# Kernel tuning notes

Hardware: AMD Instinct MI355X
Metric: run time of the kernel (lower is better)

The kernel has to match this reference:

```python
import jax, jax.numpy as jnp
from jax import lax
import numpy as np

VOCAB = 50000
EMB = 256
HID = 512
NFEAT = 2048
B, T = 128, 64


def setup_inputs() -> dict:
    key = jax.random.key(0)
    ks = jax.random.split(key, 9)
    s_e = 1.0 / np.sqrt(HID)
    return {
        "m": jax.random.randint(ks[0], (B, T), 0, VOCAB, dtype=jnp.int64) if jax.config.jax_enable_x64 else jax.random.randint(ks[0], (B, T), 0, VOCAB, dtype=jnp.int32),
        "images": jax.random.normal(ks[1], (B, NFEAT), dtype=jnp.float32),
        "emb_table": jax.random.normal(ks[2], (VOCAB, EMB), dtype=jnp.float32),
        "W_ih": jax.random.uniform(ks[3], (4 * HID, EMB), jnp.float32, -s_e, s_e),
        "W_hh": jax.random.uniform(ks[4], (4 * HID, HID), jnp.float32, -s_e, s_e),
        "b_ih": jax.random.uniform(ks[5], (4 * HID,), jnp.float32, -s_e, s_e),
        "b_hh": jax.random.uniform(ks[6], (4 * HID,), jnp.float32, -s_e, s_e),
        "W_out": jax.random.uniform(ks[7], (NFEAT, HID), jnp.float32, -s_e, s_e),
        "b_out": jax.random.uniform(ks[8], (NFEAT,), jnp.float32, -s_e, s_e),
    }


def reference(m, images, emb_table, W_ih, W_hh, b_ih, b_hh, W_out, b_out):
    # m: [B, T] int token ids. images is unused by the original forward.
    Bsz = m.shape[0]
    emb = emb_table[m]                                  # [B, T, E]
    # Precompute input projections for all steps (one big GEMM)
    x_proj = jnp.einsum("bte,ge->btg", emb, W_ih) + b_ih  # [B, T, 4H]
    x_proj = jnp.swapaxes(x_proj, 0, 1)                   # [T, B, 4H]

    h0 = jnp.zeros((Bsz, HID), dtype=emb.dtype)
    c0 = jnp.zeros((Bsz, HID), dtype=emb.dtype)

    def step(carry, xg):
        h, c = carry
        gates = xg + h @ W_hh.T + b_hh                  # [B, 4H]
        i, f, g, o = jnp.split(gates, 4, axis=-1)       # PyTorch LSTMCell gate order
        c_new = jax.nn.sigmoid(f) * c + jax.nn.sigmoid(i) * jnp.tanh(g)
        h_new = jax.nn.sigmoid(o) * jnp.tanh(c_new)
        return (h_new, c_new), None

    (h, _), _ = lax.scan(step, (h0, c0), x_proj)
    return h @ W_out.T + b_out                           # [B, NFEAT]
```

## Files before the change

kernel.cpp:

```cpp
#include <hip/hip_runtime.h>
#include <hip/hip_bf16.h>

#define BATCH 128
#define TSTEPS 64
#define EMB 256
#define HID 512
#define GATES 2048
#define NFEAT 2048

typedef __bf16 bf16_t;
typedef __attribute__((ext_vector_type(8))) __bf16 bf16x8;
typedef __attribute__((ext_vector_type(4))) float f32x4;

#define MFMA16 __builtin_amdgcn_mfma_f32_16x16x32_bf16

__device__ __forceinline__ bf16x8 frag16(const bf16_t* __restrict__ base, int row0, int stride,
                                         int k0, int lane) {
    return *(const bf16x8*)(base + (size_t)(row0 + (lane & 15)) * stride + k0 + ((lane >> 4) << 3));
}

__device__ __forceinline__ float sigm(float x) { return 1.f / (1.f + __expf(-x)); }
__device__ __forceinline__ float tanh_f(float x) { return 1.f - 2.f / (__expf(2.f * x) + 1.f); }

__device__ __forceinline__ unsigned ld_sys(const unsigned* p) {
    return __hip_atomic_load(p, __ATOMIC_RELAXED, __HIP_MEMORY_SCOPE_SYSTEM);
}
__device__ __forceinline__ void st_sys(unsigned* p, unsigned v) {
    __hip_atomic_store(p, v, __ATOMIC_RELAXED, __HIP_MEMORY_SCOPE_SYSTEM);
}
__device__ __forceinline__ void ld2_sys_v4(const void* p0, const void* p1, uint4& a, uint4& b) {
    asm volatile("global_load_dwordx4 %0, %2, off sc0 sc1\n\t"
                 "global_load_dwordx4 %1, %3, off sc0 sc1\n\t"
                 "s_waitcnt vmcnt(0)"
                 : "=&v"(a), "=&v"(b)
                 : "v"(p0), "v"(p1)
                 : "memory");
}

__device__ __forceinline__ float bflo(unsigned w) {
    return __builtin_bit_cast(float, (w & 0xffffu) << 16);
}
__device__ __forceinline__ float bfhi(unsigned w) {
    return __builtin_bit_cast(float, w & 0xffff0000u);
}
__device__ __forceinline__ unsigned f2bf(float x) {
    return (unsigned)__builtin_bit_cast(unsigned short, (bf16_t)x);
}

__global__ __launch_bounds__(256) void k_prep(
    const float* __restrict__ Wih, const float* __restrict__ Whh, const float* __restrict__ Wout,
    const float* __restrict__ bih, const float* __restrict__ bhh,
    const int* __restrict__ m, const float* __restrict__ emb_tab,
    bf16_t* __restrict__ wih_b, bf16_t* __restrict__ whh_b, bf16_t* __restrict__ wout_b,
    float* __restrict__ biassum, bf16_t* __restrict__ emb_b,
    bf16_t* __restrict__ h0, unsigned* __restrict__ cnt) {
    const int N1 = GATES * EMB;
    const int N2 = GATES * HID;
    const int N3 = NFEAT * HID;
    const int N4 = GATES;
    const int N5 = BATCH * TSTEPS * EMB;
    const int N6 = BATCH * HID;
    const int N7 = 256;
    const long total = (long)N1 + N2 + N3 + N4 + N5 + N6 + N7;
    for (long i = (long)blockIdx.x * blockDim.x + threadIdx.x; i < total;
         i += (long)gridDim.x * blockDim.x) {
        long x = i;
        if (x < N1) { wih_b[x] = (bf16_t)Wih[x]; continue; } x -= N1;
        if (x < N2) { whh_b[x] = (bf16_t)Whh[x]; continue; } x -= N2;
        if (x < N3) { wout_b[x] = (bf16_t)Wout[x]; continue; } x -= N3;
        if (x < N4) { biassum[x] = bih[x] + bhh[x]; continue; } x -= N4;
        if (x < N5) {
            int e = (int)(x & (EMB - 1));
            int rt = (int)(x >> 8);
            int t = rt >> 7, b = rt & 127;
            int tok = m[b * TSTEPS + t];
            emb_b[x] = (bf16_t)emb_tab[(size_t)tok * EMB + e];
            continue;
        } x -= N5;
        if (x < N6) { h0[x] = (bf16_t)0.f; continue; } x -= N6;
        cnt[x] = 0u;
    }
}

__global__ __launch_bounds__(256) void k_xproj(
    const bf16_t* __restrict__ A, const bf16_t* __restrict__ Wih,
    const float* __restrict__ biassum, bf16_t* __restrict__ xproj) {
    int lane = threadIdx.x & 63, w = threadIdx.x >> 6;
    int r0 = blockIdx.x * 128 + (w >> 1) * 64;
    int g0 = blockIdx.y * 128 + (w & 1) * 64;
    f32x4 acc[4][4] = {};
    #pragma unroll
    for (int k = 0; k < EMB; k += 32) {
        bf16x8 af[4], bf[4];
        #pragma unroll
        for (int i = 0; i < 4; i++) af[i] = frag16(A, r0 + 16 * i, EMB, k, lane);
        #pragma unroll
        for (int j = 0; j < 4; j++) bf[j] = frag16(Wih, g0 + 16 * j, EMB, k, lane);
        #pragma unroll
        for (int i = 0; i < 4; i++)
            #pragma unroll
            for (int j = 0; j < 4; j++)
                acc[i][j] = MFMA16(af[i], bf[j], acc[i][j], 0, 0, 0);
    }
    #pragma unroll
    for (int j = 0; j < 4; j++) {
        int g = g0 + 16 * j + (lane & 15);
        float bs = biassum[g];
        #pragma unroll
        for (int i = 0; i < 4; i++)
            #pragma unroll
            for (int r = 0; r < 4; r++) {
                int row = r0 + 16 * i + ((lane >> 4) << 2) + r;
                xproj[(size_t)row * GATES + g] = (bf16_t)(acc[i][j][r] + bs);
            }
    }
}

__global__ __launch_bounds__(512, 1) void k_rnn(
    const bf16_t* __restrict__ xp,
    const bf16_t* __restrict__ whh,
    bf16_t* __restrict__ hbuf,
    unsigned* __restrict__ cnt) {
    __shared__ __align__(16) char hstage[16384];
    __shared__ float gex[4][16][66];
    const int tid = threadIdx.x;
    const int lane = tid & 63, w = tid >> 6;
    const int group = blockIdx.x >> 3;
    const int s     = blockIdx.x & 7;
    const int g = w >> 1, hh = w & 1;

    bf16x8 Bf0[16], Bf1[16];
    {
        const bf16_t* wb = whh + (size_t)(g * HID + s * 64 + hh * 32) * HID;
        #pragma unroll
        for (int kt = 0; kt < 16; ++kt) {
            Bf0[kt] = frag16(wb, 0, HID, kt * 32, lane);
            Bf1[kt] = frag16(wb, 16, HID, kt * 32, lane);
        }
        #pragma unroll
        for (int kt = 0; kt < 16; ++kt)
            asm volatile("" : "+v"(Bf0[kt]), "+v"(Bf1[kt]));
    }

    const int r_up = tid >> 5;
    const int c0 = (tid & 31) * 2;
    float cst0 = 0.f, cst1 = 0.f;
    unsigned* myflag = cnt + group * 32;

    unsigned* hstore_base;
    {
        int j = s * 64 + c0;
        int kt = j >> 5;
        int lane_p = (((j & 31) >> 3) << 4) | r_up;
        hstore_base = (unsigned*)hbuf + (size_t)group * 4096 + kt * 256 + lane_p * 4 + ((j & 7) >> 1);
    }

    for (int t = 0; t < TSTEPS; ++t) {
        unsigned xw0, xw1, xw2, xw3;
        {
            const bf16_t* xrow = xp + ((size_t)t * BATCH + group * 16 + r_up) * GATES + s * 64 + c0;
            xw0 = *(const unsigned*)(xrow);
            xw1 = *(const unsigned*)(xrow + HID);
            xw2 = *(const unsigned*)(xrow + 2 * HID);
            xw3 = *(const unsigned*)(xrow + 3 * HID);
        }

        if (t) {
            if (tid == 0) {
                unsigned tgt = (unsigned)(8 * t);
                while (ld_sys(myflag) < tgt) __builtin_amdgcn_s_sleep(1);
            }
            __syncthreads();
            asm volatile("" ::: "memory");
        }

        {
            const char* gsrc = (const char*)hbuf + (size_t)(t & 1) * 131072
                             + (size_t)group * 16384;
            uint4 va, vb;
            ld2_sys_v4(gsrc + (size_t)tid * 16, gsrc + (size_t)(tid + 512) * 16, va, vb);
            *(uint4*)(hstage + (size_t)tid * 16) = va;
            *(uint4*)(hstage + (size_t)(tid + 512) * 16) = vb;
        }
        __syncthreads();

        f32x4 a0 = {}, a1 = {};
        {
            const bf16_t* hs = (const bf16_t*)hstage;
            #pragma unroll
            for (int kt = 0; kt < 16; ++kt) {
                bf16x8 a = *(const bf16x8*)(hs + kt * 512 + lane * 8);
                a0 = MFMA16(a, Bf0[kt], a0, 0, 0, 0);
                a1 = MFMA16(a, Bf1[kt], a1, 0, 0, 0);
            }
        }

        {
            const int jj = lane & 15, q = lane >> 4;
            #pragma unroll
            for (int rr = 0; rr < 4; ++rr) {
                gex[g][q * 4 + rr][hh * 32 + jj]      = a0[rr];
                gex[g][q * 4 + rr][hh * 32 + 16 + jj] = a1[rr];
            }
        }
        __syncthreads();

        {
            float2 gi = *(const float2*)&gex[0][r_up][c0];
            float2 gf = *(const float2*)&gex[1][r_up][c0];
            float2 gg = *(const float2*)&gex[2][r_up][c0];
            float2 go = *(const float2*)&gex[3][r_up][c0];
            float iv0 = gi.x + bflo(xw0), iv1 = gi.y + bfhi(xw0);
            float fv0 = gf.x + bflo(xw1), fv1 = gf.y + bfhi(xw1);
            float gv0 = gg.x + bflo(xw2), gv1 = gg.y + bfhi(xw2);
            float ov0 = go.x + bflo(xw3), ov1 = go.y + bfhi(xw3);
            cst0 = sigm(fv0) * cst0 + sigm(iv0) * tanh_f(gv0);
            cst1 = sigm(fv1) * cst1 + sigm(iv1) * tanh_f(gv1);
            float h0v = sigm(ov0) * tanh_f(cst0);
            float h1v = sigm(ov1) * tanh_f(cst1);
            unsigned pack = f2bf(h0v) | (f2bf(h1v) << 16);
            st_sys(hstore_base + (size_t)(((t + 1) & 1)) * 32768, pack);
        }
        __syncthreads();
        if (tid == 0 && t < TSTEPS - 1)
            __hip_atomic_fetch_add(myflag, 1u, __ATOMIC_RELAXED, __HIP_MEMORY_SCOPE_SYSTEM);
    }
}

__device__ __forceinline__ bf16x8 frag_piece(const bf16_t* hb, int group, int kt, int lane) {
    return *(const bf16x8*)(hb + (size_t)group * 8192 + kt * 512 + lane * 8);
}

__global__ __launch_bounds__(256) void k_out(
    const bf16_t* __restrict__ h,
    const bf16_t* __restrict__ Wout,
    const float* __restrict__ bout,
    float* __restrict__ out) {
    int lane = threadIdx.x & 63, w = threadIdx.x >> 6;
    int r0 = blockIdx.x * 32 + (w & 1) * 16;
    int g0 = blockIdx.y * 128 + (w >> 1) * 64;
    int group = r0 >> 4;
    f32x4 acc[4] = {};
    #pragma unroll 4
    for (int kt = 0; kt < 16; ++kt) {
        bf16x8 a = frag_piece(h, group, kt, lane);
        #pragma unroll
        for (int t = 0; t < 4; t++) {
            bf16x8 b = frag16(Wout, g0 + 16 * t, HID, kt * 32, lane);
            acc[t] = MFMA16(a, b, acc[t], 0, 0, 0);
        }
    }
    #pragma unroll
    for (int t = 0; t < 4; t++) {
        int g = g0 + 16 * t + (lane & 15);
        float bs = bout[g];
        #pragma unroll
        for (int r = 0; r < 4; r++) {
            int row = r0 + ((lane >> 4) << 2) + r;
            out[(size_t)row * NFEAT + g] = acc[t][r] + bs;
        }
    }
}

extern "C" void kernel_launch(void* const* d_in, const int* in_sizes, int n_in,
                              void* d_out, int out_size, void* d_ws, size_t ws_size,
                              hipStream_t stream) {
    const int*   m       = (const int*)d_in[0];
    const float* emb_tab = (const float*)d_in[2];
    const float* W_ih    = (const float*)d_in[3];
    const float* W_hh    = (const float*)d_in[4];
    const float* b_ih    = (const float*)d_in[5];
    const float* b_hh    = (const float*)d_in[6];
    const float* W_out   = (const float*)d_in[7];
    const float* b_out   = (const float*)d_in[8];

    char* ws = (char*)d_ws;
    bf16_t*   xpb     = (bf16_t*)  (ws + 0);
    bf16_t*   emb_b   = (bf16_t*)  (ws + 33554432);
    bf16_t*   wih_b   = (bf16_t*)  (ws + 37748736);
    bf16_t*   whh_b   = (bf16_t*)  (ws + 38797312);
    bf16_t*   wout_b  = (bf16_t*)  (ws + 40894464);
    bf16_t*   hbuf    = (bf16_t*)  (ws + 42991616);
    float*    biassum = (float*)   (ws + 43253760);
    unsigned* cnt     = (unsigned*)(ws + 43261952);

    k_prep<<<dim3(2048), dim3(256), 0, stream>>>(W_ih, W_hh, W_out, b_ih, b_hh, m, emb_tab,
                                                 wih_b, whh_b, wout_b, biassum, emb_b,
                                                 hbuf , cnt);

    k_xproj<<<dim3(64, 16), dim3(256), 0, stream>>>(emb_b, wih_b, biassum, xpb);

    k_rnn<<<dim3(64), dim3(512), 0, stream>>>(xpb, whh_b, hbuf, cnt);

    k_out<<<dim3(4, 16), dim3(256), 0, stream>>>(hbuf, wout_b, b_out, (float*)d_out);
}
```

Measured before the change: 233.6 us.

## Fuse embedding gather into xproj GEMM and use per-wave flags with triple-buffered hidden state

The embedding gather and bf16 conversion move out of the prep kernel into the input-projection GEMM, which loads fp32 rows straight from the table. This removes the intermediate emb_b buffer round trip. In the recurrent kernel, the single per-group atomic counter and block-wide barriers become per-wave step flags polled by a whole wave, and the hidden-state buffer is triple-buffered, so the trailing __syncthreads and atomic add go away. This allows producers to run further ahead. The catch is more flag polling traffic and a subtler memory-ordering protocol.

```diff
diff --git a/kernel.cpp b/kernel.cpp
--- a/kernel.cpp
+++ b/kernel.cpp
@@ -50,18 +50,15 @@
 __global__ __launch_bounds__(256) void k_prep(
     const float* __restrict__ Wih, const float* __restrict__ Whh, const float* __restrict__ Wout,
     const float* __restrict__ bih, const float* __restrict__ bhh,
-    const int* __restrict__ m, const float* __restrict__ emb_tab,
     bf16_t* __restrict__ wih_b, bf16_t* __restrict__ whh_b, bf16_t* __restrict__ wout_b,
-    float* __restrict__ biassum, bf16_t* __restrict__ emb_b,
-    bf16_t* __restrict__ h0, unsigned* __restrict__ cnt) {
+    float* __restrict__ biassum, bf16_t* __restrict__ h0, unsigned* __restrict__ wflag) {
     const int N1 = GATES * EMB;
     const int N2 = GATES * HID;
     const int N3 = NFEAT * HID;
     const int N4 = GATES;
-    const int N5 = BATCH * TSTEPS * EMB;
-    const int N6 = BATCH * HID;
-    const int N7 = 256;
-    const long total = (long)N1 + N2 + N3 + N4 + N5 + N6 + N7;
+    const int N5 = BATCH * HID;
+    const int N6 = 1024;
+    const long total = (long)N1 + N2 + N3 + N4 + N5 + N6;
     for (long i = (long)blockIdx.x * blockDim.x + threadIdx.x; i < total;
          i += (long)gridDim.x * blockDim.x) {
         long x = i;
@@ -69,31 +66,38 @@
         if (x < N2) { whh_b[x] = (bf16_t)Whh[x]; continue; } x -= N2;
         if (x < N3) { wout_b[x] = (bf16_t)Wout[x]; continue; } x -= N3;
         if (x < N4) { biassum[x] = bih[x] + bhh[x]; continue; } x -= N4;
-        if (x < N5) {
-            int e = (int)(x & (EMB - 1));
-            int rt = (int)(x >> 8);
-            int t = rt >> 7, b = rt & 127;
-            int tok = m[b * TSTEPS + t];
-            emb_b[x] = (bf16_t)emb_tab[(size_t)tok * EMB + e];
-            continue;
-        } x -= N5;
-        if (x < N6) { h0[x] = (bf16_t)0.f; continue; } x -= N6;
-        cnt[x] = 0u;
+        if (x < N5) { h0[x] = (bf16_t)0.f; continue; } x -= N5;
+        wflag[x] = 0u;
     }
 }
 
 __global__ __launch_bounds__(256) void k_xproj(
-    const bf16_t* __restrict__ A, const bf16_t* __restrict__ Wih,
-    const float* __restrict__ biassum, bf16_t* __restrict__ xproj) {
+    const int* __restrict__ m, const float* __restrict__ emb_tab,
+    const bf16_t* __restrict__ Wih, const float* __restrict__ biassum,
+    bf16_t* __restrict__ xproj) {
     int lane = threadIdx.x & 63, w = threadIdx.x >> 6;
-    int r0 = blockIdx.x * 128 + (w >> 1) * 64;
+    int t = blockIdx.x;
+    int b0 = (w >> 1) * 64;
     int g0 = blockIdx.y * 128 + (w & 1) * 64;
+    int q = lane >> 4;
+    int tok[4];
+    #pragma unroll
+    for (int i = 0; i < 4; i++)
+        tok[i] = m[(b0 + 16 * i + (lane & 15)) * TSTEPS + t];
     f32x4 acc[4][4] = {};
     #pragma unroll
     for (int k = 0; k < EMB; k += 32) {
         bf16x8 af[4], bf[4];
         #pragma unroll
-        for (int i = 0; i < 4; i++) af[i] = frag16(A, r0 + 16 * i, EMB, k, lane);
+        for (int i = 0; i < 4; i++) {
+            const float* src = emb_tab + (size_t)tok[i] * EMB + k + q * 8;
+            float4 lo = *(const float4*)(src);
+            float4 hi = *(const float4*)(src + 4);
+            bf16x8 v;
+            v[0] = (bf16_t)lo.x; v[1] = (bf16_t)lo.y; v[2] = (bf16_t)lo.z; v[3] = (bf16_t)lo.w;
+            v[4] = (bf16_t)hi.x; v[5] = (bf16_t)hi.y; v[6] = (bf16_t)hi.z; v[7] = (bf16_t)hi.w;
+            af[i] = v;
+        }
         #pragma unroll
         for (int j = 0; j < 4; j++) bf[j] = frag16(Wih, g0 + 16 * j, EMB, k, lane);
         #pragma unroll
@@ -110,7 +114,7 @@
         for (int i = 0; i < 4; i++)
             #pragma unroll
             for (int r = 0; r < 4; r++) {
-                int row = r0 + 16 * i + ((lane >> 4) << 2) + r;
+                int row = t * BATCH + b0 + 16 * i + (q << 2) + r;
                 xproj[(size_t)row * GATES + g] = (bf16_t)(acc[i][j][r] + bs);
             }
     }
@@ -120,7 +124,7 @@
     const bf16_t* __restrict__ xp,
     const bf16_t* __restrict__ whh,
     bf16_t* __restrict__ hbuf,
-    unsigned* __restrict__ cnt) {
+    unsigned* __restrict__ wflag) {
     __shared__ __align__(16) char hstage[16384];
     __shared__ float gex[4][16][66];
     const int tid = threadIdx.x;
@@ -145,16 +149,20 @@
     const int r_up = tid >> 5;
     const int c0 = (tid & 31) * 2;
     float cst0 = 0.f, cst1 = 0.f;
-    unsigned* myflag = cnt + group * 32;
-
-    unsigned* hstore_base;
+
+    const int sPoll = (w >> 1) + ((lane & 8) ? 4 : 0);
+    const unsigned* pf = wflag + (((group << 3) + sPoll) << 4) + (lane & 7);
+    unsigned* myflag = wflag + (((group << 3) + s) << 4) + w;
+
+    unsigned* hst;
     {
         int j = s * 64 + c0;
         int kt = j >> 5;
         int lane_p = (((j & 31) >> 3) << 4) | r_up;
-        hstore_base = (unsigned*)hbuf + (size_t)group * 4096 + kt * 256 + lane_p * 4 + ((j & 7) >> 1);
-    }
-
+        hst = (unsigned*)hbuf + (size_t)group * 4096 + kt * 256 + lane_p * 4 + ((j & 7) >> 1);
+    }
+
+    int parS = 0;
     for (int t = 0; t < TSTEPS; ++t) {
         unsigned xw0, xw1, xw2, xw3;
         {
@@ -166,17 +174,12 @@
         }
 
         if (t) {
-            if (tid == 0) {
-                unsigned tgt = (unsigned)(8 * t);
-                while (ld_sys(myflag) < tgt) __builtin_amdgcn_s_sleep(1);
-            }
-            __syncthreads();
-            asm volatile("" ::: "memory");
-        }
-
-        {
-            const char* gsrc = (const char*)hbuf + (size_t)(t & 1) * 131072
-                             + (size_t)group * 16384;
+            unsigned v;
+            do { v = ld_sys(pf); } while (!__all((int)(v >= (unsigned)t)));
+        }
+
+        {
+            const char* gsrc = (const char*)hbuf + (size_t)parS * 131072 + (size_t)group * 16384;
             uint4 va, vb;
             ld2_sys_v4(gsrc + (size_t)tid * 16, gsrc + (size_t)(tid + 512) * 16, va, vb);
             *(uint4*)(hstage + (size_t)tid * 16) = va;
@@ -219,11 +222,12 @@
             float h0v = sigm(ov0) * tanh_f(cst0);
             float h1v = sigm(ov1) * tanh_f(cst1);
             unsigned pack = f2bf(h0v) | (f2bf(h1v) << 16);
-            st_sys(hstore_base + (size_t)(((t + 1) & 1)) * 32768, pack);
-        }
-        __syncthreads();
-        if (tid == 0 && t < TSTEPS - 1)
-            __hip_atomic_fetch_add(myflag, 1u, __ATOMIC_RELAXED, __HIP_MEMORY_SCOPE_SYSTEM);
+            int parD = parS + 1; if (parD == 3) parD = 0;
+            st_sys(hst + (size_t)parD * 32768, pack);
+            asm volatile("s_waitcnt vmcnt(0)" ::: "memory");
+            if (lane == 0) st_sys(myflag, (unsigned)(t + 1));
+            parS = parD;
+        }
     }
 }
 
@@ -276,21 +280,20 @@
 
     char* ws = (char*)d_ws;
     bf16_t*   xpb     = (bf16_t*)  (ws + 0);
-    bf16_t*   emb_b   = (bf16_t*)  (ws + 33554432);
-    bf16_t*   wih_b   = (bf16_t*)  (ws + 37748736);
-    bf16_t*   whh_b   = (bf16_t*)  (ws + 38797312);
-    bf16_t*   wout_b  = (bf16_t*)  (ws + 40894464);
-    bf16_t*   hbuf    = (bf16_t*)  (ws + 42991616);
-    float*    biassum = (float*)   (ws + 43253760);
-    unsigned* cnt     = (unsigned*)(ws + 43261952);
-
-    k_prep<<<dim3(2048), dim3(256), 0, stream>>>(W_ih, W_hh, W_out, b_ih, b_hh, m, emb_tab,
-                                                 wih_b, whh_b, wout_b, biassum, emb_b,
-                                                 hbuf , cnt);
-
-    k_xproj<<<dim3(64, 16), dim3(256), 0, stream>>>(emb_b, wih_b, biassum, xpb);
-
-    k_rnn<<<dim3(64), dim3(512), 0, stream>>>(xpb, whh_b, hbuf, cnt);
-
-    k_out<<<dim3(4, 16), dim3(256), 0, stream>>>(hbuf, wout_b, b_out, (float*)d_out);
-}
+    bf16_t*   wih_b   = (bf16_t*)  (ws + 33554432);
+    bf16_t*   whh_b   = (bf16_t*)  (ws + 34603008);
+    bf16_t*   wout_b  = (bf16_t*)  (ws + 36700160);
+    bf16_t*   hbuf    = (bf16_t*)  (ws + 38797312);
+    float*    biassum = (float*)   (ws + 39190528);
+    unsigned* wflag   = (unsigned*)(ws + 39198720);
+
+    k_prep<<<dim3(1024), dim3(256), 0, stream>>>(W_ih, W_hh, W_out, b_ih, b_hh,
+                                                 wih_b, whh_b, wout_b, biassum,
+                                                 hbuf , wflag);
+
+    k_xproj<<<dim3(64, 16), dim3(256), 0, stream>>>(m, emb_tab, wih_b, biassum, xpb);
+
+    k_rnn<<<dim3(64), dim3(512), 0, stream>>>(xpb, whh_b, hbuf, wflag);
+
+    k_out<<<dim3(4, 16), dim3(256), 0, stream>>>(hbuf + 65536, wout_b, b_out, (float*)d_out);
+}
```

Measured after the change: 313.4 us. +34.1%, slower.

## Convert weights to bf16 on the fly and peel the zero-state first LSTM step

Applied to the files above, without the earlier changes.

Removes the prep-kernel pass that converted W_ih, W_hh and W_out to bf16 copies. Each consumer now loads fp32 weights and converts them in registers. The embedding gather is vectorised to float4, and the h0 zeroing is dropped by peeling timestep 0, where h=0 means no recurrent GEMM is needed. This cuts prep traffic and one dependent step's sync, at the cost of doubling the weight bytes read by the GEMM kernels.

```diff
diff --git a/kernel.cpp b/kernel.cpp
--- a/kernel.cpp
+++ b/kernel.cpp
@@ -18,9 +18,29 @@
                                          int k0, int lane) {
     return *(const bf16x8*)(base + (size_t)(row0 + (lane & 15)) * stride + k0 + ((lane >> 4) << 3));
 }
+__device__ __forceinline__ bf16x8 frag16f(const float* __restrict__ base, int row0, int stride,
+                                          int k0, int lane) {
+    const float* p = base + (size_t)(row0 + (lane & 15)) * stride + k0 + ((lane >> 4) << 3);
+    float4 lo = *(const float4*)p;
+    float4 hi = *(const float4*)(p + 4);
+    bf16x8 v;
+    v[0] = (bf16_t)lo.x; v[1] = (bf16_t)lo.y; v[2] = (bf16_t)lo.z; v[3] = (bf16_t)lo.w;
+    v[4] = (bf16_t)hi.x; v[5] = (bf16_t)hi.y; v[6] = (bf16_t)hi.z; v[7] = (bf16_t)hi.w;
+    return v;
+}
 
 __device__ __forceinline__ float sigm(float x) { return 1.f / (1.f + __expf(-x)); }
 __device__ __forceinline__ float tanh_f(float x) { return 1.f - 2.f / (__expf(2.f * x) + 1.f); }
+
+__device__ __forceinline__ float bflo(unsigned w) {
+    return __builtin_bit_cast(float, (w & 0xffffu) << 16);
+}
+__device__ __forceinline__ float bfhi(unsigned w) {
+    return __builtin_bit_cast(float, w & 0xffff0000u);
+}
+__device__ __forceinline__ unsigned f2bf(float x) {
+    return (unsigned)__builtin_bit_cast(unsigned short, (bf16_t)x);
+}
 
 __device__ __forceinline__ unsigned ld_sys(const unsigned* p) {
     return __hip_atomic_load(p, __ATOMIC_RELAXED, __HIP_MEMORY_SCOPE_SYSTEM);
@@ -37,54 +57,38 @@
                  : "memory");
 }
 
-__device__ __forceinline__ float bflo(unsigned w) {
-    return __builtin_bit_cast(float, (w & 0xffffu) << 16);
-}
-__device__ __forceinline__ float bfhi(unsigned w) {
-    return __builtin_bit_cast(float, w & 0xffff0000u);
-}
-__device__ __forceinline__ unsigned f2bf(float x) {
-    return (unsigned)__builtin_bit_cast(unsigned short, (bf16_t)x);
-}
-
 __global__ __launch_bounds__(256) void k_prep(
-    const float* __restrict__ Wih, const float* __restrict__ Whh, const float* __restrict__ Wout,
+    const int* __restrict__ m, const float* __restrict__ emb_tab,
     const float* __restrict__ bih, const float* __restrict__ bhh,
-    const int* __restrict__ m, const float* __restrict__ emb_tab,
-    bf16_t* __restrict__ wih_b, bf16_t* __restrict__ whh_b, bf16_t* __restrict__ wout_b,
-    float* __restrict__ biassum, bf16_t* __restrict__ emb_b,
-    bf16_t* __restrict__ h0, unsigned* __restrict__ cnt) {
-    const int N1 = GATES * EMB;
-    const int N2 = GATES * HID;
-    const int N3 = NFEAT * HID;
+    bf16_t* __restrict__ emb_b, float* __restrict__ biassum, unsigned* __restrict__ cnt) {
+    const int NG = BATCH * TSTEPS * EMB / 4;
     const int N4 = GATES;
-    const int N5 = BATCH * TSTEPS * EMB;
-    const int N6 = BATCH * HID;
-    const int N7 = 256;
-    const long total = (long)N1 + N2 + N3 + N4 + N5 + N6 + N7;
+    const int N5 = 256;
+    const long total = (long)NG + N4 + N5;
     for (long i = (long)blockIdx.x * blockDim.x + threadIdx.x; i < total;
          i += (long)gridDim.x * blockDim.x) {
         long x = i;
-        if (x < N1) { wih_b[x] = (bf16_t)Wih[x]; continue; } x -= N1;
-        if (x < N2) { whh_b[x] = (bf16_t)Whh[x]; continue; } x -= N2;
-        if (x < N3) { wout_b[x] = (bf16_t)Wout[x]; continue; } x -= N3;
-        if (x < N4) { biassum[x] = bih[x] + bhh[x]; continue; } x -= N4;
-        if (x < N5) {
-            int e = (int)(x & (EMB - 1));
-            int rt = (int)(x >> 8);
+        if (x < NG) {
+            int e4 = (int)(x & 63);
+            int rt = (int)(x >> 6);
             int t = rt >> 7, b = rt & 127;
             int tok = m[b * TSTEPS + t];
-            emb_b[x] = (bf16_t)emb_tab[(size_t)tok * EMB + e];
+            float4 v = *(const float4*)(emb_tab + (size_t)tok * EMB + e4 * 4);
+            bf16_t* dst = emb_b + (size_t)rt * EMB + e4 * 4;
+            dst[0] = (bf16_t)v.x; dst[1] = (bf16_t)v.y;
+            dst[2] = (bf16_t)v.z; dst[3] = (bf16_t)v.w;
             continue;
-        } x -= N5;
-        if (x < N6) { h0[x] = (bf16_t)0.f; continue; } x -= N6;
+        } x -= NG;
+        if (x < N4) { biassum[x] = bih[x] + bhh[x]; continue; } x -= N4;
         cnt[x] = 0u;
     }
 }
 
 __global__ __launch_bounds__(256) void k_xproj(
-    const bf16_t* __restrict__ A, const bf16_t* __restrict__ Wih,
-    const float* __restrict__ biassum, bf16_t* __restrict__ xproj) {
+    const bf16_t* __restrict__ A,
+    const float* __restrict__ Wih,
+    const float* __restrict__ biassum,
+    bf16_t* __restrict__ xproj) {
     int lane = threadIdx.x & 63, w = threadIdx.x >> 6;
     int r0 = blockIdx.x * 128 + (w >> 1) * 64;
     int g0 = blockIdx.y * 128 + (w & 1) * 64;
@@ -95,7 +99,7 @@
         #pragma unroll
         for (int i = 0; i < 4; i++) af[i] = frag16(A, r0 + 16 * i, EMB, k, lane);
         #pragma unroll
-        for (int j = 0; j < 4; j++) bf[j] = frag16(Wih, g0 + 16 * j, EMB, k, lane);
+        for (int j = 0; j < 4; j++) bf[j] = frag16f(Wih, g0 + 16 * j, EMB, k, lane);
         #pragma unroll
         for (int i = 0; i < 4; i++)
             #pragma unroll
@@ -118,8 +122,8 @@
 
 __global__ __launch_bounds__(512, 1) void k_rnn(
     const bf16_t* __restrict__ xp,
-    const bf16_t* __restrict__ whh,
-    bf16_t* __restrict__ hbuf,
+    const float* __restrict__ whh,
+    char* __restrict__ hbuf,
     unsigned* __restrict__ cnt) {
     __shared__ __align__(16) char hstage[16384];
     __shared__ float gex[4][16][66];
@@ -131,11 +135,11 @@
 
     bf16x8 Bf0[16], Bf1[16];
     {
-        const bf16_t* wb = whh + (size_t)(g * HID + s * 64 + hh * 32) * HID;
+        const float* wb = whh + (size_t)(g * HID + s * 64 + hh * 32) * HID;
         #pragma unroll
         for (int kt = 0; kt < 16; ++kt) {
-            Bf0[kt] = frag16(wb, 0, HID, kt * 32, lane);
-            Bf1[kt] = frag16(wb, 16, HID, kt * 32, lane);
+            Bf0[kt] = frag16f(wb, 0, HID, kt * 32, lane);
+            Bf1[kt] = frag16f(wb, 16, HID, kt * 32, lane);
         }
         #pragma unroll
         for (int kt = 0; kt < 16; ++kt)
@@ -147,36 +151,50 @@
     float cst0 = 0.f, cst1 = 0.f;
     unsigned* myflag = cnt + group * 32;
 
-    unsigned* hstore_base;
+    unsigned* hst;
     {
         int j = s * 64 + c0;
         int kt = j >> 5;
         int lane_p = (((j & 31) >> 3) << 4) | r_up;
-        hstore_base = (unsigned*)hbuf + (size_t)group * 4096 + kt * 256 + lane_p * 4 + ((j & 7) >> 1);
-    }
-
-    for (int t = 0; t < TSTEPS; ++t) {
+        hst = (unsigned*)hbuf + (size_t)group * 4096 + kt * 256 + lane_p * 4 + ((j & 7) >> 1);
+    }
+
+    {
+        const bf16_t* xrow = xp + ((size_t)(group * 16 + r_up)) * GATES + s * 64 + c0;
+        unsigned xw0 = *(const unsigned*)(xrow);
+        unsigned xw2 = *(const unsigned*)(xrow + 2 * HID);
+        unsigned xw3 = *(const unsigned*)(xrow + 3 * HID);
+        cst0 = sigm(bflo(xw0)) * tanh_f(bflo(xw2));
+        cst1 = sigm(bfhi(xw0)) * tanh_f(bfhi(xw2));
+        float h0v = sigm(bflo(xw3)) * tanh_f(cst0);
+        float h1v = sigm(bfhi(xw3)) * tanh_f(cst1);
+        unsigned pack = f2bf(h0v) | (f2bf(h1v) << 16);
+        st_sys(hst + 32768 , pack);
+        __syncthreads();
+        if (tid == 0)
+            __hip_atomic_fetch_add(myflag, 1u, __ATOMIC_RELAXED, __HIP_MEMORY_SCOPE_SYSTEM);
+    }
+
+    for (int t = 1; t < TSTEPS; ++t) {
         unsigned xw0, xw1, xw2, xw3;
         {
-            const bf16_t* xrow = xp + ((size_t)t * BATCH + group * 16 + r_up) * GATES + s * 64 + c0;
+            const bf16_t* xrow = xp + ((size_t)(t * BATCH + group * 16 + r_up)) * GATES
+                               + s * 64 + c0;
             xw0 = *(const unsigned*)(xrow);
             xw1 = *(const unsigned*)(xrow + HID);
             xw2 = *(const unsigned*)(xrow + 2 * HID);
             xw3 = *(const unsigned*)(xrow + 3 * HID);
         }
 
-        if (t) {
-            if (tid == 0) {
-                unsigned tgt = (unsigned)(8 * t);
-                while (ld_sys(myflag) < tgt) __builtin_amdgcn_s_sleep(1);
-            }
-            __syncthreads();
-            asm volatile("" ::: "memory");
-        }
-
-        {
-            const char* gsrc = (const char*)hbuf + (size_t)(t & 1) * 131072
-                             + (size_t)group * 16384;
+        if (tid == 0) {
+            unsigned tgt = (unsigned)(8 * t);
+            while (ld_sys(myflag) < tgt) __builtin_amdgcn_s_sleep(1);
+        }
+        __syncthreads();
+        asm volatile("" ::: "memory");
+
+        {
+            const char* gsrc = hbuf + (size_t)(t & 1) * 131072 + (size_t)group * 16384;
             uint4 va, vb;
             ld2_sys_v4(gsrc + (size_t)tid * 16, gsrc + (size_t)(tid + 512) * 16, va, vb);
             *(uint4*)(hstage + (size_t)tid * 16) = va;
@@ -219,7 +237,7 @@
             float h0v = sigm(ov0) * tanh_f(cst0);
             float h1v = sigm(ov1) * tanh_f(cst1);
             unsigned pack = f2bf(h0v) | (f2bf(h1v) << 16);
-            st_sys(hstore_base + (size_t)(((t + 1) & 1)) * 32768, pack);
+            st_sys(hst + (size_t)(((t + 1) & 1)) * 32768, pack);
         }
         __syncthreads();
         if (tid == 0 && t < TSTEPS - 1)
@@ -233,7 +251,7 @@
 
 __global__ __launch_bounds__(256) void k_out(
     const bf16_t* __restrict__ h,
-    const bf16_t* __restrict__ Wout,
+    const float* __restrict__ Wout,
     const float* __restrict__ bout,
     float* __restrict__ out) {
     int lane = threadIdx.x & 63, w = threadIdx.x >> 6;
@@ -246,7 +264,7 @@
         bf16x8 a = frag_piece(h, group, kt, lane);
         #pragma unroll
         for (int t = 0; t < 4; t++) {
-            bf16x8 b = frag16(Wout, g0 + 16 * t, HID, kt * 32, lane);
+            bf16x8 b = frag16f(Wout, g0 + 16 * t, HID, kt * 32, lane);
             acc[t] = MFMA16(a, b, acc[t], 0, 0, 0);
         }
     }
@@ -277,20 +295,16 @@
     char* ws = (char*)d_ws;
     bf16_t*   xpb     = (bf16_t*)  (ws + 0);
     bf16_t*   emb_b   = (bf16_t*)  (ws + 33554432);
-    bf16_t*   wih_b   = (bf16_t*)  (ws + 37748736);
-    bf16_t*   whh_b   = (bf16_t*)  (ws + 38797312);
-    bf16_t*   wout_b  = (bf16_t*)  (ws + 40894464);
-    bf16_t*   hbuf    = (bf16_t*)  (ws + 42991616);
-    float*    biassum = (float*)   (ws + 43253760);
-    unsigned* cnt     = (unsigned*)(ws + 43261952);
-
-    k_prep<<<dim3(2048), dim3(256), 0, stream>>>(W_ih, W_hh, W_out, b_ih, b_hh, m, emb_tab,
-                                                 wih_b, whh_b, wout_b, biassum, emb_b,
-                                                 hbuf , cnt);
-
-    k_xproj<<<dim3(64, 16), dim3(256), 0, stream>>>(emb_b, wih_b, biassum, xpb);
-
-    k_rnn<<<dim3(64), dim3(512), 0, stream>>>(xpb, whh_b, hbuf, cnt);
-
-    k_out<<<dim3(4, 16), dim3(256), 0, stream>>>(hbuf, wout_b, b_out, (float*)d_out);
-}
+    char*     hbuf    = (char*)    (ws + 37748736);
+    float*    biassum = (float*)   (ws + 38010880);
+    unsigned* cnt     = (unsigned*)(ws + 38019072);
+
+    k_prep<<<dim3(1024), dim3(256), 0, stream>>>(m, emb_tab, b_ih, b_hh, emb_b, biassum, cnt);
+
+    k_xproj<<<dim3(64, 16), dim3(256), 0, stream>>>(emb_b, W_ih, biassum, xpb);
+
+    k_rnn<<<dim3(64), dim3(512), 0, stream>>>(xpb, W_hh, hbuf, cnt);
+
+    k_out<<<dim3(4, 16), dim3(256), 0, stream>>>((const bf16_t*)hbuf, W_out, b_out,
+                                                 (float*)d_out);
+}
```

Result: slower. 271.0 us (+16.0%).
